# Kernel tuning notes

Measured on AMD Instinct MI355X. Metric: run time of the kernel, lower is better.

Reference implementation:

```python
import jax, jax.numpy as jnp
import numpy as np

NQ = 7  # start_qubits
QCSTEP = [4, 1, 2, 1, 1, 1]


def _ry(psi, theta, w):
    """Apply RY(theta) on wire w. psi: [B] + [2]*NQ, wire w at axis w+1."""
    ax = w + 1
    c = jnp.cos(theta / 2)
    s = jnp.sin(theta / 2)
    a0 = jax.lax.index_in_dim(psi, 0, ax, keepdims=False)
    a1 = jax.lax.index_in_dim(psi, 1, ax, keepdims=False)
    return jnp.stack([c * a0 - s * a1, s * a0 + c * a1], axis=ax)


def _cnot(psi, c, t):
    """Apply CNOT(control=c, target=t)."""
    axc, axt = c + 1, t + 1
    s0 = jax.lax.index_in_dim(psi, 0, axc, keepdims=False)
    s1 = jax.lax.index_in_dim(psi, 1, axc, keepdims=False)
    axt2 = axt if axt < axc else axt - 1  # target axis after removing control axis
    s1 = jnp.flip(s1, axis=axt2)
    return jnp.stack([s0, s1], axis=axc)


def _simulate(x, QCs, QPs, QF):
    B = x.shape[0]
    # AmplitudeEmbedding with normalize=True (real input -> real state, wire 0 = MSB)
    psi = x / jnp.linalg.norm(x, axis=1, keepdims=True)
    psi = psi.reshape((B,) + (2,) * NQ)
    for j in range(6):
        sq = NQ - j
        qc, qp, step = QCs[j], QPs[j], QCSTEP[j]
        idx = 0
        for i in range(sq):
            psi = _ry(psi, qc[idx], i); idx += 1
        for i in range(sq):
            if i == 0:
                psi = _ry(psi, qc[idx], 0); idx += 1
                psi = _cnot(psi, sq - 1, 0)
                psi = _ry(psi, qc[idx], 0); idx += 1
            else:
                w = sq - i
                psi = _ry(psi, qc[idx], w); idx += 1
                psi = _cnot(psi, w - 1, w)
                psi = _ry(psi, qc[idx], w); idx += 1
        for i in range(sq):
            psi = _ry(psi, qc[idx], i); idx += 1
        control, controled = 0, step
        for i in range(sq):
            psi = _ry(psi, qc[idx], controled); idx += 1
            psi = _cnot(psi, control, controled)
            psi = _ry(psi, qc[idx], controled); idx += 1
            control = controled
            controled = (controled + step) % sq
        pidx = 0
        for i in range(sq - 1):
            psi = _ry(psi, qp[pidx], i + 1); pidx += 1
            psi = _cnot(psi, i, i + 1)
            psi = _ry(psi, qp[pidx], i + 1); pidx += 1
    psi = _ry(psi, QF[0], 0)
    # probs on wire 0: marginalize amplitudes^2 over wires 1..6 -> [B, 2]
    return jnp.sum(psi * psi, axis=tuple(range(2, NQ + 1)))


def setup_inputs() -> dict:
    key = jax.random.key(0)
    ks = jax.random.split(key, 15)
    B = 262144
    inp = {"x": jax.random.normal(ks[0], (B, 2 ** NQ), dtype=jnp.float32)}
    qc_sizes = [42, 36, 30, 24, 18, 12]
    qp_sizes = [12, 10, 8, 6, 4, 2]
    for j in range(6):
        inp[f"QC{j + 1}"] = jax.random.normal(ks[1 + j], (qc_sizes[j],), dtype=jnp.float32)
        inp[f"QP{j + 1}"] = jax.random.normal(ks[7 + j], (qp_sizes[j],), dtype=jnp.float32)
    inp["QF"] = jax.random.normal(ks[13], (1,), dtype=jnp.float32)
    return inp


def reference(x, QC1, QC2, QC3, QC4, QC5, QC6, QP1, QP2, QP3, QP4, QP5, QP6, QF):
    QCs = [QC1, QC2, QC3, QC4, QC5, QC6]
    QPs = [QP1, QP2, QP3, QP4, QP5, QP6]
    return _simulate(x, QCs, QPs, QF)
```

## Files before the change

### kernel.cpp

```cpp
#include <hip/hip_runtime.h>

typedef _Float16 f16x8 __attribute__((ext_vector_type(8)));
typedef float f32x4 __attribute__((ext_vector_type(4)));


__device__ __forceinline__ void ry_gate(float& a0, float& a1, int w, int lane,
                                        float c, float s) {
  if (w == 0) {
    float n0 = c * a0 - s * a1;
    float n1 = s * a0 + c * a1;
    a0 = n0; a1 = n1;
  } else {
    int m = 1 << (6 - w);
    float p0 = __shfl_xor(a0, m);
    float p1 = __shfl_xor(a1, m);
    if (lane & m) {
      a0 = s * p0 + c * a0;
      a1 = s * p1 + c * a1;
    } else {
      a0 = c * a0 - s * p0;
      a1 = c * a1 - s * p1;
    }
  }
}

__device__ __forceinline__ void cnot_gate(float& a0, float& a1, int c, int t,
                                          int lane) {
  if (c == 0) {
    int mt = 1 << (6 - t);
    a1 = __shfl_xor(a1, mt);
  } else if (t == 0) {
    int mc = 1 << (6 - c);
    if (lane & mc) { float tmp = a0; a0 = a1; a1 = tmp; }
  } else {
    int mc = 1 << (6 - c), mt = 1 << (6 - t);
    float p0 = __shfl_xor(a0, mt);
    float p1 = __shfl_xor(a1, mt);
    if (lane & mc) { a0 = p0; a1 = p1; }
  }
}

__global__ __launch_bounds__(64) void basis_kernel(
    const float* __restrict__ qc1, const float* __restrict__ qc2,
    const float* __restrict__ qc3, const float* __restrict__ qc4,
    const float* __restrict__ qc5, const float* __restrict__ qc6,
    const float* __restrict__ qp1, const float* __restrict__ qp2,
    const float* __restrict__ qp3, const float* __restrict__ qp4,
    const float* __restrict__ qp5, const float* __restrict__ qp6,
    const float* __restrict__ qf, _Float16* __restrict__ wt) {
  __shared__ float2 cs[208];
  int lane = threadIdx.x;

  {
    const float* arrs[13] = {qc1, qp1, qc2, qp2, qc3, qp3, qc4,
                             qp4, qc5, qp5, qc6, qp6, qf};
    const int sizes[13] = {42, 12, 36, 10, 30, 8, 24, 6, 18, 4, 12, 2, 1};
    for (int t = lane; t < 205; t += 64) {
      int base = 0; float ang = 0.f;
#pragma unroll
      for (int s2 = 0; s2 < 13; ++s2) {
        if (t >= base && t < base + sizes[s2]) ang = arrs[s2][t - base];
        base += sizes[s2];
      }
      float h = 0.5f * ang;
      cs[t] = make_float2(cosf(h), sinf(h));
    }
  }
  __syncthreads();

  int k = blockIdx.x;
  float a0 = ((k >> 6) == 0 && (k & 63) == lane) ? 1.0f : 0.0f;
  float a1 = ((k >> 6) == 1 && (k & 63) == lane) ? 1.0f : 0.0f;
  int g = 0;

  const int qcstep[6] = {4, 1, 2, 1, 1, 1};
#define RYG(w)                                        \
  { float2 csv = cs[g++]; ry_gate(a0, a1, (w), lane, csv.x, csv.y); }
#define CNG(c, t) cnot_gate(a0, a1, (c), (t), lane);

#pragma unroll
  for (int j = 0; j < 6; ++j) {
    int sq = 7 - j;
    int step = qcstep[j];
    for (int i = 0; i < sq; ++i) { RYG(i); }
    for (int i = 0; i < sq; ++i) {
      if (i == 0) { RYG(0); CNG(sq - 1, 0); RYG(0); }
      else { int w = sq - i; RYG(w); CNG(w - 1, w); RYG(w); }
    }
    for (int i = 0; i < sq; ++i) { RYG(i); }
    int control = 0, controled = step;
    for (int i = 0; i < sq; ++i) {
      RYG(controled); CNG(control, controled); RYG(controled);
      control = controled; controled = (controled + step) % sq;
    }
    for (int i = 0; i < sq - 1; ++i) { RYG(i + 1); CNG(i, i + 1); RYG(i + 1); }
  }
  RYG(0);

  wt[lane * 128 + k] = (_Float16)a0;
  wt[(lane + 64) * 128 + k] = (_Float16)a1;
#undef RYG
#undef CNG
}

__global__ __launch_bounds__(256, 4) void qcnn_gemm(
    const float* __restrict__ X, const _Float16* __restrict__ wt,
    float* __restrict__ out, int M) {
  __shared__ uint4 ldsbuf[2048];
  char* lds = (char*)ldsbuf;
  int tid = threadIdx.x;

#pragma unroll
  for (int it = 0; it < 8; ++it) {
    int idx16 = it * 2048 + tid * 8;
    int n = idx16 >> 7;
    int k2 = (idx16 & 127) * 2;
    uint4 v = *(const uint4*)(wt + idx16);
    *(uint4*)(lds + n * 256 + (k2 ^ ((n & 7) << 4))) = v;
  }
  __syncthreads();

  int wave = tid >> 6, lane = tid & 63;
  int rb0 = blockIdx.x * 128 + wave * 32;
  if (rb0 >= M) return;
  int lr = lane & 15;
  int lk = (lane >> 4) * 8;
  int swz = (lane & 7) << 4;
  int grp = lane >> 4;

  for (int mt = 0; mt < 2; ++mt) {
    int rb = rb0 + mt * 16;
    const float* xp = X + (size_t)(rb + lr) * 128 + lk;

    float4 v0[4], v1[4];
#pragma unroll
    for (int ks = 0; ks < 4; ++ks) {
      v0[ks] = *(const float4*)(xp + ks * 32);
      v1[ks] = *(const float4*)(xp + ks * 32 + 4);
    }

    f32x4 acc[8];
#pragma unroll
    for (int nf = 0; nf < 8; ++nf) acc[nf] = (f32x4){0.f, 0.f, 0.f, 0.f};

#pragma unroll
    for (int ks = 0; ks < 4; ++ks) {
      f16x8 a;
      a[0] = (_Float16)v0[ks].x; a[1] = (_Float16)v0[ks].y;
      a[2] = (_Float16)v0[ks].z; a[3] = (_Float16)v0[ks].w;
      a[4] = (_Float16)v1[ks].x; a[5] = (_Float16)v1[ks].y;
      a[6] = (_Float16)v1[ks].z; a[7] = (_Float16)v1[ks].w;
      int boff = (ks * 64 + lk * 2) ^ swz;
#pragma unroll
      for (int nf = 0; nf < 8; ++nf) {
        int n = nf * 16 + lr;
        f16x8 b = *(const f16x8*)(lds + n * 256 + boff);
        acc[nf] = __builtin_amdgcn_mfma_f32_16x16x32_f16(a, b, acc[nf], 0, 0, 0);
      }
    }

    float s0[4], s1[4];
#pragma unroll
    for (int r = 0; r < 4; ++r) {
      float t0 = 0.f, t1 = 0.f;
#pragma unroll
      for (int nf = 0; nf < 4; ++nf) t0 += acc[nf][r] * acc[nf][r];
#pragma unroll
      for (int nf = 4; nf < 8; ++nf) t1 += acc[nf][r] * acc[nf][r];
      s0[r] = t0; s1[r] = t1;
    }
#pragma unroll
    for (int d = 1; d < 16; d <<= 1) {
#pragma unroll
      for (int r = 0; r < 4; ++r) {
        s0[r] += __shfl_xor(s0[r], d);
        s1[r] += __shfl_xor(s1[r], d);
      }
    }
    int row = rb + grp * 4;
#pragma unroll
    for (int r = 0; r < 4; ++r) {
      if ((lane & 15) == r) {
        float inv = 1.0f / (s0[r] + s1[r]);
        *(float2*)(out + (size_t)(row + r) * 2) =
            make_float2(s0[r] * inv, s1[r] * inv);
      }
    }
  }
}

extern "C" void kernel_launch(void* const* d_in, const int* in_sizes, int n_in,
                              void* d_out, int out_size, void* d_ws,
                              size_t ws_size, hipStream_t stream) {
  const float* X = (const float*)d_in[0];
  _Float16* wt = (_Float16*)d_ws;

  basis_kernel<<<128, 64, 0, stream>>>(
       (const float*)d_in[1],  (const float*)d_in[3],
       (const float*)d_in[5],  (const float*)d_in[7],
       (const float*)d_in[9],  (const float*)d_in[11],
       (const float*)d_in[2],  (const float*)d_in[4],
       (const float*)d_in[6],  (const float*)d_in[8],
       (const float*)d_in[10],  (const float*)d_in[12],
       (const float*)d_in[13], wt);

  int M = in_sizes[0] / 128;
  qcnn_gemm<<<(M + 127) / 128, 256, 0, stream>>>(X, wt, (float*)d_out, M);
}
```

Before: 43.22 us.

## Prefetch X tiles before LDS load and software-pipeline row tiles

The first X tile load is issued before the weight matrix is staged into LDS, so the global read overlaps the LDS fill and barrier. Each wave now handles four 16-row tiles strided by 64 rows and prefetches the next tile's registers while running MFMAs on the current one. Blocks cover 256 rows, which halves the grid and halves the redundant per-block LDS weight loads. The fp16 conversion uses packed round-toward-zero conversions, which changes rounding slightly. The prefetch buffers raise register pressure.

Result: no change. 42.58 us (-1.5%).

```diff
diff --git a/kernel.cpp b/kernel.cpp
--- a/kernel.cpp
+++ b/kernel.cpp
@@ -109,81 +109,105 @@
   __shared__ uint4 ldsbuf[2048];
   char* lds = (char*)ldsbuf;
   int tid = threadIdx.x;
+  int wave = tid >> 6, lane = tid & 63;
+  int lr = lane & 15;
+  int g = lane >> 4;
+  int lk = g * 8;
+  int swz = (lane & 7) << 4;
+
+  size_t base0 = (size_t)blockIdx.x * 256 + wave * 16;
+
+  float4 v0[4], v1[4];
+  if (base0 < (size_t)M) {
+    const float* xp = X + (base0 + lr) * 128 + lk;
+#pragma unroll
+    for (int ks = 0; ks < 4; ++ks) {
+      v0[ks] = *(const float4*)(xp + ks * 32);
+      v1[ks] = *(const float4*)(xp + ks * 32 + 4);
+    }
+  }
 
 #pragma unroll
   for (int it = 0; it < 8; ++it) {
     int idx16 = it * 2048 + tid * 8;
     int n = idx16 >> 7;
     int k2 = (idx16 & 127) * 2;
-    uint4 v = *(const uint4*)(wt + idx16);
-    *(uint4*)(lds + n * 256 + (k2 ^ ((n & 7) << 4))) = v;
+    uint4 w = *(const uint4*)(wt + idx16);
+    *(uint4*)(lds + n * 256 + (k2 ^ ((n & 7) << 4))) = w;
   }
   __syncthreads();
 
-  int wave = tid >> 6, lane = tid & 63;
-  int rb0 = blockIdx.x * 128 + wave * 32;
-  if (rb0 >= M) return;
-  int lr = lane & 15;
-  int lk = (lane >> 4) * 8;
-  int swz = (lane & 7) << 4;
-  int grp = lane >> 4;
-
-  for (int mt = 0; mt < 2; ++mt) {
-    int rb = rb0 + mt * 16;
-    const float* xp = X + (size_t)(rb + lr) * 128 + lk;
-
-    float4 v0[4], v1[4];
-#pragma unroll
-    for (int ks = 0; ks < 4; ++ks) {
-      v0[ks] = *(const float4*)(xp + ks * 32);
-      v1[ks] = *(const float4*)(xp + ks * 32 + 4);
-    }
-
-    f32x4 acc[8];
-#pragma unroll
-    for (int nf = 0; nf < 8; ++nf) acc[nf] = (f32x4){0.f, 0.f, 0.f, 0.f};
-
-#pragma unroll
-    for (int ks = 0; ks < 4; ++ks) {
-      f16x8 a;
-      a[0] = (_Float16)v0[ks].x; a[1] = (_Float16)v0[ks].y;
-      a[2] = (_Float16)v0[ks].z; a[3] = (_Float16)v0[ks].w;
-      a[4] = (_Float16)v1[ks].x; a[5] = (_Float16)v1[ks].y;
-      a[6] = (_Float16)v1[ks].z; a[7] = (_Float16)v1[ks].w;
-      int boff = (ks * 64 + lk * 2) ^ swz;
-#pragma unroll
-      for (int nf = 0; nf < 8; ++nf) {
-        int n = nf * 16 + lr;
-        f16x8 b = *(const f16x8*)(lds + n * 256 + boff);
-        acc[nf] = __builtin_amdgcn_mfma_f32_16x16x32_f16(a, b, acc[nf], 0, 0, 0);
-      }
-    }
-
-    float s0[4], s1[4];
-#pragma unroll
-    for (int r = 0; r < 4; ++r) {
-      float t0 = 0.f, t1 = 0.f;
-#pragma unroll
-      for (int nf = 0; nf < 4; ++nf) t0 += acc[nf][r] * acc[nf][r];
-#pragma unroll
-      for (int nf = 4; nf < 8; ++nf) t1 += acc[nf][r] * acc[nf][r];
-      s0[r] = t0; s1[r] = t1;
-    }
-#pragma unroll
-    for (int d = 1; d < 16; d <<= 1) {
+#pragma unroll
+  for (int t = 0; t < 4; ++t) {
+    size_t rb = base0 + (size_t)t * 64;
+    if (rb < (size_t)M) {
+      f16x8 a[4];
+#pragma unroll
+      for (int ks = 0; ks < 4; ++ks) {
+        auto p0 = __builtin_amdgcn_cvt_pkrtz(v0[ks].x, v0[ks].y);
+        auto p1 = __builtin_amdgcn_cvt_pkrtz(v0[ks].z, v0[ks].w);
+        auto p2 = __builtin_amdgcn_cvt_pkrtz(v1[ks].x, v1[ks].y);
+        auto p3 = __builtin_amdgcn_cvt_pkrtz(v1[ks].z, v1[ks].w);
+        f16x8 f;
+        f[0] = (_Float16)p0[0]; f[1] = (_Float16)p0[1];
+        f[2] = (_Float16)p1[0]; f[3] = (_Float16)p1[1];
+        f[4] = (_Float16)p2[0]; f[5] = (_Float16)p2[1];
+        f[6] = (_Float16)p3[0]; f[7] = (_Float16)p3[1];
+        a[ks] = f;
+      }
+
+      if (t < 3) {
+        size_t rn = base0 + (size_t)(t + 1) * 64;
+        if (rn < (size_t)M) {
+          const float* xp = X + (rn + lr) * 128 + lk;
+#pragma unroll
+          for (int ks = 0; ks < 4; ++ks) {
+            v0[ks] = *(const float4*)(xp + ks * 32);
+            v1[ks] = *(const float4*)(xp + ks * 32 + 4);
+          }
+        }
+      }
+
+      f32x4 acc[8];
+#pragma unroll
+      for (int nf = 0; nf < 8; ++nf) acc[nf] = (f32x4){0.f, 0.f, 0.f, 0.f};
+
+#pragma unroll
+      for (int ks = 0; ks < 4; ++ks) {
+        int boff = (ks * 64 + lk * 2) ^ swz;
+#pragma unroll
+        for (int nf = 0; nf < 8; ++nf) {
+          f16x8 b = *(const f16x8*)(lds + (nf * 16 + lr) * 256 + boff);
+          acc[nf] = __builtin_amdgcn_mfma_f32_16x16x32_f16(a[ks], b, acc[nf], 0, 0, 0);
+        }
+      }
+
+      float s0[4], s1[4];
 #pragma unroll
       for (int r = 0; r < 4; ++r) {
-        s0[r] += __shfl_xor(s0[r], d);
-        s1[r] += __shfl_xor(s1[r], d);
-      }
-    }
-    int row = rb + grp * 4;
-#pragma unroll
-    for (int r = 0; r < 4; ++r) {
-      if ((lane & 15) == r) {
-        float inv = 1.0f / (s0[r] + s1[r]);
-        *(float2*)(out + (size_t)(row + r) * 2) =
-            make_float2(s0[r] * inv, s1[r] * inv);
+        float t0 = 0.f, t1 = 0.f;
+#pragma unroll
+        for (int nf = 0; nf < 4; ++nf) t0 += acc[nf][r] * acc[nf][r];
+#pragma unroll
+        for (int nf = 4; nf < 8; ++nf) t1 += acc[nf][r] * acc[nf][r];
+        s0[r] = t0; s1[r] = t1;
+      }
+#pragma unroll
+      for (int d = 1; d < 16; d <<= 1) {
+#pragma unroll
+        for (int r = 0; r < 4; ++r) {
+          s0[r] += __shfl_xor(s0[r], d);
+          s1[r] += __shfl_xor(s1[r], d);
+        }
+      }
+      size_t row = rb + g * 4;
+#pragma unroll
+      for (int r = 0; r < 4; ++r) {
+        if ((lane & 15) == r) {
+          float inv = 1.0f / (s0[r] + s1[r]);
+          *(float2*)(out + (row + r) * 2) =
+              make_float2(s0[r] * inv, s1[r] * inv);
+        }
       }
     }
   }
@@ -205,5 +229,6 @@
        (const float*)d_in[13], wt);
 
   int M = in_sizes[0] / 128;
-  qcnn_gemm<<<(M + 127) / 128, 256, 0, stream>>>(X, wt, (float*)d_out, M);
-}
+  int nblk = (M + 255) / 256;
+  qcnn_gemm<<<nblk, 256, 0, stream>>>(X, wt, (float*)d_out, M);
+}
```

## Switch GEMM to 32x32x16 MFMA with pre-laid-out B and transpose-reduce epilogue

Applied to the files above, without the earlier changes.

The basis kernel now writes the unitary into a layout that matches the 32x32x16 MFMA B-operand lane order, so the GEMM can copy it to LDS linearly and read it without swizzling. The GEMM switches from 16x16x32 to 32x32x16 MFMAs, doubles rows per block with a two-stage software prefetch of X, and uses packed RTZ conversion to f16. The epilogue replaces the full butterfly reductions with a transpose-style shuffle reduction in which each lane ends up owning one output element. The risks are higher register pressure from 64 accumulator floats plus prefetch buffers, RTZ rounding instead of round-to-nearest, and the removal of the row bound check for M not divisible by 256.

Result: slower. 44.46 us (+2.9%).

```diff
diff --git a/kernel.cpp b/kernel.cpp
--- a/kernel.cpp
+++ b/kernel.cpp
@@ -1,7 +1,7 @@
 #include <hip/hip_runtime.h>
 
 typedef _Float16 f16x8 __attribute__((ext_vector_type(8)));
-typedef float f32x4 __attribute__((ext_vector_type(4)));
+typedef float f32x16 __attribute__((ext_vector_type(16)));
 
 
 __device__ __forceinline__ void ry_gate(float& a0, float& a1, int w, int lane,
@@ -71,11 +71,11 @@
   int k = blockIdx.x;
   float a0 = ((k >> 6) == 0 && (k & 63) == lane) ? 1.0f : 0.0f;
   float a1 = ((k >> 6) == 1 && (k & 63) == lane) ? 1.0f : 0.0f;
-  int g = 0;
+  int gi = 0;
 
   const int qcstep[6] = {4, 1, 2, 1, 1, 1};
 #define RYG(w)                                        \
-  { float2 csv = cs[g++]; ry_gate(a0, a1, (w), lane, csv.x, csv.y); }
+  { float2 csv = cs[gi++]; ry_gate(a0, a1, (w), lane, csv.x, csv.y); }
 #define CNG(c, t) cnot_gate(a0, a1, (c), (t), lane);
 
 #pragma unroll
@@ -96,95 +96,120 @@
     for (int i = 0; i < sq - 1; ++i) { RYG(i + 1); CNG(i, i + 1); RYG(i + 1); }
   }
   RYG(0);
-
-  wt[lane * 128 + k] = (_Float16)a0;
-  wt[(lane + 64) * 128 + k] = (_Float16)a1;
 #undef RYG
 #undef CNG
+
+  {
+    int ks = k >> 4, hi2 = (k >> 3) & 1, j = k & 7;
+    int nfa = lane >> 5, c5 = lane & 31;
+    wt[(ks * 4 + nfa) * 512 + hi2 * 256 + c5 * 8 + j] = (_Float16)a0;
+    wt[(ks * 4 + 2 + nfa) * 512 + hi2 * 256 + c5 * 8 + j] = (_Float16)a1;
+  }
 }
 
 __global__ __launch_bounds__(256, 4) void qcnn_gemm(
     const float* __restrict__ X, const _Float16* __restrict__ wt,
     float* __restrict__ out, int M) {
   __shared__ uint4 ldsbuf[2048];
-  char* lds = (char*)ldsbuf;
   int tid = threadIdx.x;
-
-#pragma unroll
-  for (int it = 0; it < 8; ++it) {
-    int idx16 = it * 2048 + tid * 8;
-    int n = idx16 >> 7;
-    int k2 = (idx16 & 127) * 2;
-    uint4 v = *(const uint4*)(wt + idx16);
-    *(uint4*)(lds + n * 256 + (k2 ^ ((n & 7) << 4))) = v;
+  int wave = tid >> 6, lane = tid & 63;
+  int r5 = lane & 31;
+  int hi = lane >> 5;
+
+  {
+    const uint4* wv = (const uint4*)wt;
+#pragma unroll
+    for (int c = 0; c < 8; ++c) ldsbuf[c * 256 + tid] = wv[c * 256 + tid];
   }
   __syncthreads();
 
-  int wave = tid >> 6, lane = tid & 63;
-  int rb0 = blockIdx.x * 128 + wave * 32;
-  if (rb0 >= M) return;
-  int lr = lane & 15;
-  int lk = (lane >> 4) * 8;
-  int swz = (lane & 7) << 4;
-  int grp = lane >> 4;
-
-  for (int mt = 0; mt < 2; ++mt) {
-    int rb = rb0 + mt * 16;
-    const float* xp = X + (size_t)(rb + lr) * 128 + lk;
-
-    float4 v0[4], v1[4];
-#pragma unroll
-    for (int ks = 0; ks < 4; ++ks) {
-      v0[ks] = *(const float4*)(xp + ks * 32);
-      v1[ks] = *(const float4*)(xp + ks * 32 + 4);
-    }
-
-    f32x4 acc[8];
-#pragma unroll
-    for (int nf = 0; nf < 8; ++nf) acc[nf] = (f32x4){0.f, 0.f, 0.f, 0.f};
-
-#pragma unroll
-    for (int ks = 0; ks < 4; ++ks) {
+  const char* bbase = (const char*)ldsbuf + lane * 16;
+
+#pragma unroll
+  for (int t = 0; t < 2; ++t) {
+    int rb = blockIdx.x * 256 + wave * 32 + t * 128;
+    const float* xp = X + (size_t)(rb + r5) * 128 + hi * 8;
+
+    float4 f0[8], f1[8];
+    f0[0] = *(const float4*)(xp);          f1[0] = *(const float4*)(xp + 4);
+    f0[1] = *(const float4*)(xp + 16);     f1[1] = *(const float4*)(xp + 20);
+
+    f32x16 acc[4];
+#pragma unroll
+    for (int nf = 0; nf < 4; ++nf)
+#pragma unroll
+      for (int e = 0; e < 16; ++e) acc[nf][e] = 0.f;
+
+#pragma unroll
+    for (int ks = 0; ks < 8; ++ks) {
+      if (ks + 2 < 8) {
+        f0[ks + 2] = *(const float4*)(xp + (ks + 2) * 16);
+        f1[ks + 2] = *(const float4*)(xp + (ks + 2) * 16 + 4);
+      }
+      auto p0 = __builtin_amdgcn_cvt_pkrtz(f0[ks].x, f0[ks].y);
+      auto p1 = __builtin_amdgcn_cvt_pkrtz(f0[ks].z, f0[ks].w);
+      auto p2 = __builtin_amdgcn_cvt_pkrtz(f1[ks].x, f1[ks].y);
+      auto p3 = __builtin_amdgcn_cvt_pkrtz(f1[ks].z, f1[ks].w);
       f16x8 a;
-      a[0] = (_Float16)v0[ks].x; a[1] = (_Float16)v0[ks].y;
-      a[2] = (_Float16)v0[ks].z; a[3] = (_Float16)v0[ks].w;
-      a[4] = (_Float16)v1[ks].x; a[5] = (_Float16)v1[ks].y;
-      a[6] = (_Float16)v1[ks].z; a[7] = (_Float16)v1[ks].w;
-      int boff = (ks * 64 + lk * 2) ^ swz;
-#pragma unroll
-      for (int nf = 0; nf < 8; ++nf) {
-        int n = nf * 16 + lr;
-        f16x8 b = *(const f16x8*)(lds + n * 256 + boff);
-        acc[nf] = __builtin_amdgcn_mfma_f32_16x16x32_f16(a, b, acc[nf], 0, 0, 0);
+      a[0] = (_Float16)p0[0]; a[1] = (_Float16)p0[1];
+      a[2] = (_Float16)p1[0]; a[3] = (_Float16)p1[1];
+      a[4] = (_Float16)p2[0]; a[5] = (_Float16)p2[1];
+      a[6] = (_Float16)p3[0]; a[7] = (_Float16)p3[1];
+#pragma unroll
+      for (int nf = 0; nf < 4; ++nf) {
+        f16x8 b = *(const f16x8*)(bbase + ((ks * 4 + nf) << 10));
+        acc[nf] = __builtin_amdgcn_mfma_f32_32x32x16_f16(a, b, acc[nf], 0, 0, 0);
       }
     }
 
-    float s0[4], s1[4];
-#pragma unroll
-    for (int r = 0; r < 4; ++r) {
-      float t0 = 0.f, t1 = 0.f;
-#pragma unroll
-      for (int nf = 0; nf < 4; ++nf) t0 += acc[nf][r] * acc[nf][r];
-#pragma unroll
-      for (int nf = 4; nf < 8; ++nf) t1 += acc[nf][r] * acc[nf][r];
-      s0[r] = t0; s1[r] = t1;
-    }
-#pragma unroll
-    for (int d = 1; d < 16; d <<= 1) {
-#pragma unroll
-      for (int r = 0; r < 4; ++r) {
-        s0[r] += __shfl_xor(s0[r], d);
-        s1[r] += __shfl_xor(s1[r], d);
-      }
-    }
-    int row = rb + grp * 4;
-#pragma unroll
-    for (int r = 0; r < 4; ++r) {
-      if ((lane & 15) == r) {
-        float inv = 1.0f / (s0[r] + s1[r]);
-        *(float2*)(out + (size_t)(row + r) * 2) =
-            make_float2(s0[r] * inv, s1[r] * inv);
-      }
+    float v[32];
+#pragma unroll
+    for (int rg = 0; rg < 16; ++rg) {
+      v[rg * 2 + 0] = acc[0][rg] * acc[0][rg] + acc[1][rg] * acc[1][rg];
+      v[rg * 2 + 1] = acc[2][rg] * acc[2][rg] + acc[3][rg] * acc[3][rg];
+    }
+    int kb = lane & 1;
+    float n1[16];
+#pragma unroll
+    for (int i = 0; i < 16; ++i) {
+      float snd = kb ? v[2 * i] : v[2 * i + 1];
+      float rcv = __shfl_xor(snd, 1);
+      n1[i] = (kb ? v[2 * i + 1] : v[2 * i]) + rcv;
+    }
+    int kb2 = (lane >> 1) & 1;
+    float n2[8];
+#pragma unroll
+    for (int i = 0; i < 8; ++i) {
+      float snd = kb2 ? n1[2 * i] : n1[2 * i + 1];
+      float rcv = __shfl_xor(snd, 2);
+      n2[i] = (kb2 ? n1[2 * i + 1] : n1[2 * i]) + rcv;
+    }
+    int kb3 = (lane >> 2) & 1;
+    float n3[4];
+#pragma unroll
+    for (int i = 0; i < 4; ++i) {
+      float snd = kb3 ? n2[2 * i] : n2[2 * i + 1];
+      float rcv = __shfl_xor(snd, 4);
+      n3[i] = (kb3 ? n2[2 * i + 1] : n2[2 * i]) + rcv;
+    }
+    int kb4 = (lane >> 3) & 1;
+    float n4[2];
+#pragma unroll
+    for (int i = 0; i < 2; ++i) {
+      float snd = kb4 ? n3[2 * i] : n3[2 * i + 1];
+      float rcv = __shfl_xor(snd, 8);
+      n4[i] = (kb4 ? n3[2 * i + 1] : n3[2 * i]) + rcv;
+    }
+    int kb5 = (lane >> 4) & 1;
+    {
+      float snd = kb5 ? n4[0] : n4[1];
+      float rcv = __shfl_xor(snd, 16);
+      float S = (kb5 ? n4[1] : n4[0]) + rcv;
+      float T = __shfl_xor(S, 1);
+      float prob = S / (S + T);
+      int reg = (lane >> 1) & 15;
+      int row = (reg & 3) + 8 * (reg >> 2) + 4 * hi;
+      out[(size_t)(rb + row) * 2 + (lane & 1)] = prob;
     }
   }
 }
@@ -205,5 +230,6 @@
        (const float*)d_in[13], wt);
 
   int M = in_sizes[0] / 128;
-  qcnn_gemm<<<(M + 127) / 128, 256, 0, stream>>>(X, wt, (float*)d_out, M);
-}
+  int nblk = (M + 255) / 256;
+  qcnn_gemm<<<nblk, 256, 0, stream>>>(X, wt, (float*)d_out, M);
+}
```
